# Optimization experiments

Measured on AMD Instinct MI355X. Metric: run time of the kernel, lower is better.

The kernel has to match this reference:

```python
import jax, jax.numpy as jnp
import numpy as np

NEG_INF = -1e30

def setup_inputs() -> dict:
    key = jax.random.key(0)
    ks = jax.random.split(key, 8)
    N, E = 4096, 16384
    Fn, Fe, Dn, De = 128, 64, 128, 64
    # xavier_uniform bound = sqrt(6/(fan_in+fan_out)); for 1-D params torch treats shape as (1, len)
    bn = np.sqrt(6.0 / (Fn + Dn))
    be = np.sqrt(6.0 / (Fe + De))
    return {
        "node_features": jax.random.normal(ks[0], (N, Fn), dtype=jnp.float32),
        "edge_features": jax.random.normal(ks[1], (E, Fe), dtype=jnp.float32),
        "adjacency_matrix": jax.random.randint(ks[2], (N, N), 0, 2, dtype=jnp.int32),
        "edge_adjacency_matrix": jax.random.randint(ks[3], (E, N), 0, 2, dtype=jnp.int32),
        "weight_node": jax.random.uniform(ks[4], (Fn, Dn), minval=-bn, maxval=bn, dtype=jnp.float32),
        "weight_edge": jax.random.uniform(ks[5], (Fe, De), minval=-be, maxval=be, dtype=jnp.float32),
        "parameter_vector_node": jax.random.uniform(ks[6], (2 * Dn,), minval=-1.0, maxval=1.0, dtype=jnp.float32),
        "parameter_vector_edge": jax.random.uniform(ks[7], (Dn + De,), minval=-1.0, maxval=1.0, dtype=jnp.float32),
    }


def reference(node_features, edge_features, adjacency_matrix, edge_adjacency_matrix,
              weight_node, weight_edge, parameter_vector_node, parameter_vector_edge):
    lrelu = jax.nn.leaky_relu  # default negative_slope=0.01, matches torch LeakyReLU
    Dn = weight_node.shape[1]

    h = node_features @ weight_node          # [N, Dn]
    he = edge_features @ weight_edge         # [E, De]

    # ---- node-level attention ----
    a_self, a_neigh = parameter_vector_node[:Dn], parameter_vector_node[Dn:]
    # score[i, j] = leaky_relu(a . cat(h_i, h_j)) for j a neighbor of i (adjacency[j, i] > 0)
    s_n = lrelu((h @ a_self)[:, None] + (h @ a_neigh)[None, :])   # [N, N]
    mask_n = adjacency_matrix.T > 0                                # [N, N], row i = neighbors of i
    coef_n = jax.nn.softmax(jnp.where(mask_n, s_n, NEG_INF), axis=1)
    coef_n = jnp.where(mask_n, coef_n, 0.0)
    deg_n = jnp.sum(mask_n, axis=1).astype(h.dtype)                # [N]
    means_n = (coef_n @ node_features) / deg_n[:, None]            # [N, Fn] (torch.mean divides by deg)
    out_n = lrelu(means_n @ weight_node)                           # [N, Dn]

    # ---- edge-level attention ----
    b_self, b_edge = parameter_vector_edge[:Dn], parameter_vector_edge[Dn:]
    s_e = lrelu((h @ b_self)[:, None] + (he @ b_edge)[None, :])    # [N, E]
    mask_e = edge_adjacency_matrix.T > 0                           # [N, E]
    coef_e = jax.nn.softmax(jnp.where(mask_e, s_e, NEG_INF), axis=1)
    coef_e = jnp.where(mask_e, coef_e, 0.0)
    deg_e = jnp.sum(mask_e, axis=1).astype(h.dtype)
    means_e = (coef_e @ edge_features) / deg_e[:, None]            # [N, Fe]
    out_e = lrelu(means_e @ weight_edge)                           # [N, De]

    return jnp.concatenate([out_n, out_e], axis=1)                 # [N, Dn+De]
```

## Files before the change

### kernel.cpp

```cpp
#include <hip/hip_runtime.h>

typedef short bf16x8 __attribute__((ext_vector_type(8)));
typedef float f32x4 __attribute__((ext_vector_type(4)));

#define N_NODES 4096
#define N_EDGES 16384
#define FN 128
#define FE 64
#define NJS 8
#define EJS 16

__device__ __forceinline__ float lrelu(float x) { return x >= 0.f ? x : 0.01f * x; }
__device__ __forceinline__ unsigned short f2bf(float f) {
    unsigned int x = __float_as_uint(f);
    return (unsigned short)((x + 0x7fffu + ((x >> 16) & 1u)) >> 16);
}

__global__ __launch_bounds__(256) void k_node_proj(
    const float* __restrict__ nf, const float* __restrict__ Wn,
    const float* __restrict__ pvn, const float* __restrict__ pve,
    float* __restrict__ alpha, float* __restrict__ beta, float* __restrict__ gamma) {
    __shared__ float row[4][FN];
    const int wv = threadIdx.x >> 6, ln = threadIdx.x & 63;
    const int i = blockIdx.x * 4 + wv;
    float2 r2 = *(const float2*)(nf + (size_t)i * FN + ln * 2);
    row[wv][ln * 2] = r2.x; row[wv][ln * 2 + 1] = r2.y;
    __syncthreads();
    float h0 = 0.f, h1 = 0.f;
#pragma unroll 8
    for (int k = 0; k < FN; ++k) {
        float nv = row[wv][k];
        float2 w2 = *(const float2*)(Wn + (size_t)k * FN + ln * 2);
        h0 = fmaf(nv, w2.x, h0); h1 = fmaf(nv, w2.y, h1);
    }
    float2 as = *(const float2*)(pvn + ln * 2);
    float2 an = *(const float2*)(pvn + FN + ln * 2);
    float2 bs = *(const float2*)(pve + ln * 2);
    float pa = h0 * as.x + h1 * as.y;
    float pb = h0 * an.x + h1 * an.y;
    float pg = h0 * bs.x + h1 * bs.y;
#pragma unroll
    for (int off = 32; off > 0; off >>= 1) {
        pa += __shfl_down(pa, off, 64);
        pb += __shfl_down(pb, off, 64);
        pg += __shfl_down(pg, off, 64);
    }
    if (ln == 0) { alpha[i] = pa; beta[i] = pb; gamma[i] = pg; }
}

__global__ __launch_bounds__(256) void k_edge_proj(
    const float* __restrict__ ef, const float* __restrict__ We,
    const float* __restrict__ pve, float* __restrict__ betaE) {
    __shared__ float row[4][FE];
    const int wv = threadIdx.x >> 6, ln = threadIdx.x & 63;
    const int e = blockIdx.x * 4 + wv;
    row[wv][ln] = ef[(size_t)e * FE + ln];
    __syncthreads();
    float h = 0.f;
#pragma unroll 8
    for (int k = 0; k < FE; ++k)
        h = fmaf(row[wv][k], We[(size_t)k * FE + ln], h);
    float p = h * pve[FN + ln];
#pragma unroll
    for (int off = 32; off > 0; off >>= 1) p += __shfl_down(p, off, 64);
    if (ln == 0) betaE[e] = p;
}

__global__ __launch_bounds__(256) void k_maxes(
    const float* __restrict__ beta, const float* __restrict__ betaE,
    float* __restrict__ maxes) {
    const float* src = blockIdx.x == 0 ? beta : betaE;
    const int n = blockIdx.x == 0 ? N_NODES : N_EDGES;
    float m = -3.0e38f;
    for (int t = threadIdx.x; t < n; t += 256) m = fmaxf(m, src[t]);
#pragma unroll
    for (int off = 32; off > 0; off >>= 1) m = fmaxf(m, __shfl_down(m, off, 64));
    __shared__ float sm[4];
    if ((threadIdx.x & 63) == 0) sm[threadIdx.x >> 6] = m;
    __syncthreads();
    if (threadIdx.x == 0)
        maxes[blockIdx.x] = fmaxf(fmaxf(sm[0], sm[1]), fmaxf(sm[2], sm[3]));
}

__global__ __launch_bounds__(256) void k_prep(
    const float* __restrict__ src, unsigned short* __restrict__ dst,
    const int J, const int F) {
    __shared__ float tile[64][65];
    const int t = threadIdx.x;
    const int j0 = blockIdx.x * 64, f0 = blockIdx.y * 64;
#pragma unroll
    for (int p = 0; p < 4; ++p) {
        int j = (t >> 4) + p * 16;
        float4 v = *(const float4*)(src + (size_t)(j0 + j) * F + f0 + (t & 15) * 4);
        tile[j][(t & 15) * 4 + 0] = v.x;
        tile[j][(t & 15) * 4 + 1] = v.y;
        tile[j][(t & 15) * 4 + 2] = v.z;
        tile[j][(t & 15) * 4 + 3] = v.w;
    }
    __syncthreads();
#pragma unroll
    for (int p = 0; p < 2; ++p) {
        int f = (t >> 3) + p * 32;
        int c = t & 7;
        bf16x8 v;
#pragma unroll
        for (int e = 0; e < 8; ++e) v[e] = (short)f2bf(tile[c * 8 + e][f]);
        *(bf16x8*)(dst + (size_t)(f0 + f) * J + j0 + c * 8) = v;
    }
}

__global__ __launch_bounds__(256) void k_node_att(
    const unsigned short* __restrict__ Xt,
    const int* __restrict__ adj,
    const float* __restrict__ alpha, const float* __restrict__ beta,
    const float* __restrict__ maxes,
    float* __restrict__ accP, float* __restrict__ zP, float* __restrict__ degP) {
    __shared__ unsigned short xlds[128 * 64];
    __shared__ unsigned short wlds[4 * 512];
    __shared__ float bb[512];
    __shared__ float zred[8][32];
    __shared__ float dred[8][32];
    const int t = threadIdx.x;
    const int i0 = blockIdx.x * 32;
    const int bj = blockIdx.y;
    const int j0 = bj * (N_NODES / NJS);
    const int il = t & 31;
    const int jg = t >> 5;
    const float a_i = alpha[i0 + il];
    const float m_i = lrelu(a_i + maxes[0]);
    if (t < 128) *(float4*)&bb[t * 4] = *(const float4*)(beta + j0 + t * 4);
    const int l = t & 63, wid = t >> 6;
    const int wm = wid >> 1, wn = wid & 1;
    const int l15 = l & 15, l4 = l >> 4;
    const int sf = t >> 3, sc = t & 7;
    const int xswz = (sc ^ (sf & 7)) * 8;
    const int wdst = ((jg >> 2) * 2 + (il >> 4)) * 512 + ((il & 15) + 16 * (jg & 3)) * 8;
    f32x4 acc[4] = {{0,0,0,0},{0,0,0,0},{0,0,0,0},{0,0,0,0}};
    float zacc = 0.f, dacc = 0.f;
    __syncthreads();
    for (int ks = 0; ks < 8; ++ks) {
        const int jb = ks * 64;
        const int* mp = adj + (size_t)(j0 + jb + jg * 8) * N_NODES + i0 + il;
        int mk[8];
#pragma unroll
        for (int e = 0; e < 8; ++e) mk[e] = mp[(size_t)e * N_NODES];
        const unsigned short* xs = Xt + (size_t)sf * N_NODES + j0 + jb + sc * 8;
        bf16x8 xv0 = *(const bf16x8*)(xs);
        bf16x8 xv1 = *(const bf16x8*)(xs + (size_t)32 * N_NODES);
        bf16x8 xv2 = *(const bf16x8*)(xs + (size_t)64 * N_NODES);
        bf16x8 xv3 = *(const bf16x8*)(xs + (size_t)96 * N_NODES);
        bf16x8 wfrag;
#pragma unroll
        for (int e = 0; e < 8; ++e) {
            float s = lrelu(a_i + bb[jb + jg * 8 + e]);
            float w = mk[e] > 0 ? __expf(s - m_i) : 0.f;
            zacc += w;
            dacc += (mk[e] > 0) ? 1.f : 0.f;
            wfrag[e] = (short)f2bf(w);
        }
        __syncthreads();
        *(bf16x8*)&xlds[(sf +  0) * 64 + xswz] = xv0;
        *(bf16x8*)&xlds[(sf + 32) * 64 + xswz] = xv1;
        *(bf16x8*)&xlds[(sf + 64) * 64 + xswz] = xv2;
        *(bf16x8*)&xlds[(sf + 96) * 64 + xswz] = xv3;
        *(bf16x8*)&wlds[wdst] = wfrag;
        __syncthreads();
#pragma unroll
        for (int kb = 0; kb < 2; ++kb) {
            bf16x8 b = *(const bf16x8*)&wlds[(kb * 2 + wn) * 512 + l * 8];
#pragma unroll
            for (int mi = 0; mi < 4; ++mi) {
                const int fr = wm * 64 + mi * 16 + l15;
                bf16x8 a = *(const bf16x8*)&xlds[fr * 64 + (((kb * 4 + l4) ^ (fr & 7)) * 8)];
                acc[mi] = __builtin_amdgcn_mfma_f32_16x16x32_bf16(a, b, acc[mi], 0, 0, 0);
            }
        }
    }
    zred[jg][il] = zacc;
    dred[jg][il] = dacc;
    __syncthreads();
    if (t < 32) {
        float z = 0.f, d = 0.f;
#pragma unroll
        for (int g = 0; g < 8; ++g) { z += zred[g][t]; d += dred[g][t]; }
        zP[bj * N_NODES + i0 + t] = z;
        degP[bj * N_NODES + i0 + t] = d;
    }
    const int ig = i0 + wn * 16 + l15;
#pragma unroll
    for (int mi = 0; mi < 4; ++mi) {
        const int fg = wm * 64 + mi * 16 + l4 * 4;
        *(f32x4*)(accP + ((size_t)bj * N_NODES + ig) * FN + fg) = acc[mi];
    }
}

__global__ __launch_bounds__(256) void k_edge_att(
    const unsigned short* __restrict__ Xt,
    const int* __restrict__ eadj,
    const float* __restrict__ gamma, const float* __restrict__ betaE,
    const float* __restrict__ maxes,
    float* __restrict__ accP, float* __restrict__ zP, float* __restrict__ degP) {
    __shared__ unsigned short xlds[64 * 32];
    __shared__ unsigned short wlds[4 * 512];
    __shared__ float bb[1024];
    __shared__ float zred[4][64];
    __shared__ float dred[4][64];
    const int t = threadIdx.x;
    const int i0 = blockIdx.x * 64;
    const int bj = blockIdx.y;
    const int j0 = bj * (N_EDGES / EJS);
    const int il = t & 63;
    const int jg = t >> 6;
    const float g_i = gamma[i0 + il];
    const float m_i = lrelu(g_i + maxes[1]);
    *(float4*)&bb[t * 4] = *(const float4*)(betaE + j0 + t * 4);
    const int l = t & 63, wid = t >> 6;
    const int wm = wid >> 1, wn = wid & 1;
    const int l15 = l & 15, l4 = l >> 4;
    const int sf = t >> 2, sc = t & 3;
    const unsigned short* xsrc = Xt + (size_t)sf * N_EDGES + j0 + sc * 8;
    const int xdst = sf * 32 + ((sc ^ (sf & 3)) * 8);
    const int wdst = (il >> 4) * 512 + ((il & 15) + 16 * jg) * 8;
    const int ar0 = (wm * 2) * 16 + l15;
    const int ar1 = (wm * 2 + 1) * 16 + l15;
    const int aad0 = ar0 * 32 + ((l4 ^ (ar0 & 3)) * 8);
    const int aad1 = ar1 * 32 + ((l4 ^ (ar1 & 3)) * 8);
    const int bad0 = (wn * 2) * 512 + l * 8;
    const int bad1 = (wn * 2 + 1) * 512 + l * 8;
    f32x4 acc00 = {0,0,0,0}, acc01 = {0,0,0,0}, acc10 = {0,0,0,0}, acc11 = {0,0,0,0};
    float zacc = 0.f, dacc = 0.f;
    __syncthreads();
    for (int ks = 0; ks < 32; ++ks) {
        const int jb = ks * 32;
        const int* mp = eadj + (size_t)(j0 + jb + jg * 8) * N_NODES + i0 + il;
        int mk[8];
#pragma unroll
        for (int e = 0; e < 8; ++e) mk[e] = mp[(size_t)e * N_NODES];
        bf16x8 xv = *(const bf16x8*)(xsrc + jb);
        bf16x8 wfrag;
#pragma unroll
        for (int e = 0; e < 8; ++e) {
            float s = lrelu(g_i + bb[jb + jg * 8 + e]);
            float w = mk[e] > 0 ? __expf(s - m_i) : 0.f;
            zacc += w;
            dacc += (mk[e] > 0) ? 1.f : 0.f;
            wfrag[e] = (short)f2bf(w);
        }
        __syncthreads();
        *(bf16x8*)&xlds[xdst] = xv;
        *(bf16x8*)&wlds[wdst] = wfrag;
        __syncthreads();
        bf16x8 a0 = *(const bf16x8*)&xlds[aad0];
        bf16x8 a1 = *(const bf16x8*)&xlds[aad1];
        bf16x8 b0 = *(const bf16x8*)&wlds[bad0];
        bf16x8 b1 = *(const bf16x8*)&wlds[bad1];
        acc00 = __builtin_amdgcn_mfma_f32_16x16x32_bf16(a0, b0, acc00, 0, 0, 0);
        acc01 = __builtin_amdgcn_mfma_f32_16x16x32_bf16(a0, b1, acc01, 0, 0, 0);
        acc10 = __builtin_amdgcn_mfma_f32_16x16x32_bf16(a1, b0, acc10, 0, 0, 0);
        acc11 = __builtin_amdgcn_mfma_f32_16x16x32_bf16(a1, b1, acc11, 0, 0, 0);
    }
    zred[jg][il] = zacc;
    dred[jg][il] = dacc;
    __syncthreads();
    if (t < 64) {
        float z = zred[0][t] + zred[1][t] + zred[2][t] + zred[3][t];
        float d = dred[0][t] + dred[1][t] + dred[2][t] + dred[3][t];
        zP[bj * N_NODES + i0 + t] = z;
        degP[bj * N_NODES + i0 + t] = d;
    }
    const size_t obase = (size_t)bj * N_NODES;
    {
        int ig0 = i0 + (wn * 2) * 16 + l15;
        int ig1 = i0 + (wn * 2 + 1) * 16 + l15;
        int fg0 = (wm * 2) * 16 + l4 * 4;
        int fg1 = (wm * 2 + 1) * 16 + l4 * 4;
        *(f32x4*)(accP + (obase + ig0) * FE + fg0) = acc00;
        *(f32x4*)(accP + (obase + ig1) * FE + fg0) = acc01;
        *(f32x4*)(accP + (obase + ig0) * FE + fg1) = acc10;
        *(f32x4*)(accP + (obase + ig1) * FE + fg1) = acc11;
    }
}

__global__ __launch_bounds__(256) void k_node_out(
    const float* __restrict__ accP, const float* __restrict__ zP,
    const float* __restrict__ degP, const float* __restrict__ Wn,
    float* __restrict__ out) {
    __shared__ float ml[4][FN];
    const int wv = threadIdx.x >> 6, ln = threadIdx.x & 63;
    const int i = blockIdx.x * 4 + wv;
    float s0 = 0.f, s1 = 0.f;
#pragma unroll
    for (int js = 0; js < NJS; ++js) {
        float2 v = *(const float2*)(accP + ((size_t)js * N_NODES + i) * FN + ln * 2);
        s0 += v.x; s1 += v.y;
    }
    float z = 0.f, d = 0.f;
#pragma unroll
    for (int js = 0; js < NJS; ++js) { z += zP[js * N_NODES + i]; d += degP[js * N_NODES + i]; }
    float zd = z * d;
    float inv = zd > 0.f ? 1.f / zd : 0.f;
    ml[wv][ln * 2] = s0 * inv; ml[wv][ln * 2 + 1] = s1 * inv;
    __syncthreads();
    float o0 = 0.f, o1 = 0.f;
#pragma unroll 8
    for (int k = 0; k < FN; ++k) {
        float mvv = ml[wv][k];
        float2 w2 = *(const float2*)(Wn + (size_t)k * FN + ln * 2);
        o0 = fmaf(mvv, w2.x, o0); o1 = fmaf(mvv, w2.y, o1);
    }
    out[(size_t)i * 192 + ln * 2] = lrelu(o0);
    out[(size_t)i * 192 + ln * 2 + 1] = lrelu(o1);
}

__global__ __launch_bounds__(256) void k_edge_out(
    const float* __restrict__ accP, const float* __restrict__ zP,
    const float* __restrict__ degP, const float* __restrict__ We,
    float* __restrict__ out) {
    __shared__ float ml[4][FE];
    const int wv = threadIdx.x >> 6, ln = threadIdx.x & 63;
    const int i = blockIdx.x * 4 + wv;
    float s = 0.f;
#pragma unroll
    for (int js = 0; js < EJS; ++js)
        s += accP[((size_t)js * N_NODES + i) * FE + ln];
    float z = 0.f, d = 0.f;
#pragma unroll
    for (int js = 0; js < EJS; ++js) { z += zP[js * N_NODES + i]; d += degP[js * N_NODES + i]; }
    float zd = z * d;
    float inv = zd > 0.f ? 1.f / zd : 0.f;
    ml[wv][ln] = s * inv;
    __syncthreads();
    float o = 0.f;
#pragma unroll 8
    for (int k = 0; k < FE; ++k)
        o = fmaf(ml[wv][k], We[(size_t)k * FE + ln], o);
    out[(size_t)i * 192 + 128 + ln] = lrelu(o);
}

extern "C" void kernel_launch(void* const* d_in, const int* in_sizes, int n_in,
                              void* d_out, int out_size, void* d_ws, size_t ws_size,
                              hipStream_t stream) {
    (void)in_sizes; (void)n_in; (void)out_size; (void)ws_size;
    const float* nf   = (const float*)d_in[0];
    const float* ef   = (const float*)d_in[1];
    const int*   adj  = (const int*)d_in[2];
    const int*   eadj = (const int*)d_in[3];
    const float* Wn   = (const float*)d_in[4];
    const float* We   = (const float*)d_in[5];
    const float* pvn  = (const float*)d_in[6];
    const float* pve  = (const float*)d_in[7];
    float* out = (float*)d_out;

    float* alpha = (float*)d_ws;
    float* beta  = alpha + 4096;
    float* gamma = beta + 4096;
    float* betaE = gamma + 4096;
    float* maxes = betaE + 16384;
    unsigned short* XtN = (unsigned short*)(maxes + 64);
    unsigned short* XtE = XtN + (size_t)FN * N_NODES;
    float* accN = (float*)(XtE + (size_t)FE * N_EDGES);
    float* zN   = accN + (size_t)NJS * N_NODES * FN;
    float* degN = zN + (size_t)NJS * N_NODES;
    float* accE = degN + (size_t)NJS * N_NODES;
    float* zE   = accE + (size_t)EJS * N_NODES * FE;
    float* degE = zE + (size_t)EJS * N_NODES;

    k_node_proj<<<N_NODES / 4, 256, 0, stream>>>(nf, Wn, pvn, pve, alpha, beta, gamma);
    k_edge_proj<<<N_EDGES / 4, 256, 0, stream>>>(ef, We, pve, betaE);
    k_maxes<<<2, 256, 0, stream>>>(beta, betaE, maxes);
    k_prep<<<dim3(N_NODES / 64, FN / 64), 256, 0, stream>>>(nf, XtN, N_NODES, FN);
    k_prep<<<dim3(N_EDGES / 64, FE / 64), 256, 0, stream>>>(ef, XtE, N_EDGES, FE);
    k_node_att<<<dim3(N_NODES / 32, NJS), 256, 0, stream>>>(XtN, adj, alpha, beta, maxes, accN, zN, degN);
    k_edge_att<<<dim3(N_NODES / 64, EJS), 256, 0, stream>>>(XtE, eadj, gamma, betaE, maxes, accE, zE, degE);
    k_node_out<<<N_NODES / 4, 256, 0, stream>>>(accN, zN, degN, Wn, out);
    k_edge_out<<<N_NODES / 4, 256, 0, stream>>>(accE, zE, degE, We, out);
}
```

Baseline: 165.4 us.

## Double-buffer LDS and prefetch next tile in node and edge attention kernels

Both attention kernels now use double-buffered shared-memory tiles and issue the global loads for the next K-step (adjacency mask and transposed features) before the barrier. This removes one __syncthreads per iteration and lets global memory latency overlap with the MFMA work. The edge kernel also widens its K-step from 32 to 64 edges, halving the iteration count and doing twice the MFMAs per barrier. In exchange it uses more LDS and registers, which may lower occupancy. The degree count now sums the raw mask values, which assumes the mask holds only 0 or 1.

```diff
diff --git a/kernel.cpp b/kernel.cpp
--- a/kernel.cpp
+++ b/kernel.cpp
@@ -115,8 +115,8 @@
     const float* __restrict__ alpha, const float* __restrict__ beta,
     const float* __restrict__ maxes,
     float* __restrict__ accP, float* __restrict__ zP, float* __restrict__ degP) {
-    __shared__ unsigned short xlds[128 * 64];
-    __shared__ unsigned short wlds[4 * 512];
+    __shared__ unsigned short xlds[2][128 * 64];
+    __shared__ unsigned short wlds[2][4 * 512];
     __shared__ float bb[512];
     __shared__ float zred[8][32];
     __shared__ float dred[8][32];
@@ -137,44 +137,59 @@
     const int wdst = ((jg >> 2) * 2 + (il >> 4)) * 512 + ((il & 15) + 16 * (jg & 3)) * 8;
     f32x4 acc[4] = {{0,0,0,0},{0,0,0,0},{0,0,0,0},{0,0,0,0}};
     float zacc = 0.f, dacc = 0.f;
-    __syncthreads();
+
+    const int* mp0 = adj + (size_t)(j0 + jg * 8) * N_NODES + i0 + il;
+    const unsigned short* xs0 = Xt + (size_t)sf * N_NODES + j0 + sc * 8;
+
+    int mk[8];
+#pragma unroll
+    for (int e = 0; e < 8; ++e) mk[e] = mp0[(size_t)e * N_NODES];
+    bf16x8 xv0 = *(const bf16x8*)(xs0);
+    bf16x8 xv1 = *(const bf16x8*)(xs0 + (size_t)32 * N_NODES);
+    bf16x8 xv2 = *(const bf16x8*)(xs0 + (size_t)64 * N_NODES);
+    bf16x8 xv3 = *(const bf16x8*)(xs0 + (size_t)96 * N_NODES);
+    __syncthreads();
+
+    int buf = 0;
     for (int ks = 0; ks < 8; ++ks) {
         const int jb = ks * 64;
-        const int* mp = adj + (size_t)(j0 + jb + jg * 8) * N_NODES + i0 + il;
-        int mk[8];
-#pragma unroll
-        for (int e = 0; e < 8; ++e) mk[e] = mp[(size_t)e * N_NODES];
-        const unsigned short* xs = Xt + (size_t)sf * N_NODES + j0 + jb + sc * 8;
-        bf16x8 xv0 = *(const bf16x8*)(xs);
-        bf16x8 xv1 = *(const bf16x8*)(xs + (size_t)32 * N_NODES);
-        bf16x8 xv2 = *(const bf16x8*)(xs + (size_t)64 * N_NODES);
-        bf16x8 xv3 = *(const bf16x8*)(xs + (size_t)96 * N_NODES);
         bf16x8 wfrag;
 #pragma unroll
         for (int e = 0; e < 8; ++e) {
             float s = lrelu(a_i + bb[jb + jg * 8 + e]);
             float w = mk[e] > 0 ? __expf(s - m_i) : 0.f;
             zacc += w;
-            dacc += (mk[e] > 0) ? 1.f : 0.f;
+            dacc += (float)mk[e];
             wfrag[e] = (short)f2bf(w);
         }
+        *(bf16x8*)&xlds[buf][(sf +  0) * 64 + xswz] = xv0;
+        *(bf16x8*)&xlds[buf][(sf + 32) * 64 + xswz] = xv1;
+        *(bf16x8*)&xlds[buf][(sf + 64) * 64 + xswz] = xv2;
+        *(bf16x8*)&xlds[buf][(sf + 96) * 64 + xswz] = xv3;
+        *(bf16x8*)&wlds[buf][wdst] = wfrag;
+        if (ks + 1 < 8) {
+            const int jbn = jb + 64;
+            const int* mp = mp0 + (size_t)jbn * N_NODES;
+#pragma unroll
+            for (int e = 0; e < 8; ++e) mk[e] = mp[(size_t)e * N_NODES];
+            const unsigned short* xs = xs0 + jbn;
+            xv0 = *(const bf16x8*)(xs);
+            xv1 = *(const bf16x8*)(xs + (size_t)32 * N_NODES);
+            xv2 = *(const bf16x8*)(xs + (size_t)64 * N_NODES);
+            xv3 = *(const bf16x8*)(xs + (size_t)96 * N_NODES);
+        }
         __syncthreads();
-        *(bf16x8*)&xlds[(sf +  0) * 64 + xswz] = xv0;
-        *(bf16x8*)&xlds[(sf + 32) * 64 + xswz] = xv1;
-        *(bf16x8*)&xlds[(sf + 64) * 64 + xswz] = xv2;
-        *(bf16x8*)&xlds[(sf + 96) * 64 + xswz] = xv3;
-        *(bf16x8*)&wlds[wdst] = wfrag;
-        __syncthreads();
 #pragma unroll
         for (int kb = 0; kb < 2; ++kb) {
-            bf16x8 b = *(const bf16x8*)&wlds[(kb * 2 + wn) * 512 + l * 8];
+            bf16x8 b = *(const bf16x8*)&wlds[buf][(kb * 2 + wn) * 512 + l * 8];
 #pragma unroll
             for (int mi = 0; mi < 4; ++mi) {
                 const int fr = wm * 64 + mi * 16 + l15;
-                bf16x8 a = *(const bf16x8*)&xlds[fr * 64 + (((kb * 4 + l4) ^ (fr & 7)) * 8)];
+                bf16x8 a = *(const bf16x8*)&xlds[buf][fr * 64 + (((kb * 4 + l4) ^ (fr & 7)) * 8)];
                 acc[mi] = __builtin_amdgcn_mfma_f32_16x16x32_bf16(a, b, acc[mi], 0, 0, 0);
             }
         }
+        buf ^= 1;
     }
     zred[jg][il] = zacc;
     dred[jg][il] = dacc;
@@ -200,8 +215,8 @@
     const float* __restrict__ gamma, const float* __restrict__ betaE,
     const float* __restrict__ maxes,
     float* __restrict__ accP, float* __restrict__ zP, float* __restrict__ degP) {
-    __shared__ unsigned short xlds[64 * 32];
-    __shared__ unsigned short wlds[4 * 512];
+    __shared__ unsigned short xlds[2][64 * 64];
+    __shared__ unsigned short wlds[2][8 * 512];
     __shared__ float bb[1024];
     __shared__ float zred[4][64];
     __shared__ float dred[4][64];
@@ -218,46 +233,68 @@
     const int wm = wid >> 1, wn = wid & 1;
     const int l15 = l & 15, l4 = l >> 4;
     const int sf = t >> 2, sc = t & 3;
+    const int xd0 = sf * 64 + ((sc       ^ (sf & 7)) * 8);
+    const int xd1 = sf * 64 + (((sc + 4) ^ (sf & 7)) * 8);
     const unsigned short* xsrc = Xt + (size_t)sf * N_EDGES + j0 + sc * 8;
-    const int xdst = sf * 32 + ((sc ^ (sf & 3)) * 8);
-    const int wdst = (il >> 4) * 512 + ((il & 15) + 16 * jg) * 8;
-    const int ar0 = (wm * 2) * 16 + l15;
-    const int ar1 = (wm * 2 + 1) * 16 + l15;
-    const int aad0 = ar0 * 32 + ((l4 ^ (ar0 & 3)) * 8);
-    const int aad1 = ar1 * 32 + ((l4 ^ (ar1 & 3)) * 8);
-    const int bad0 = (wn * 2) * 512 + l * 8;
-    const int bad1 = (wn * 2 + 1) * 512 + l * 8;
-    f32x4 acc00 = {0,0,0,0}, acc01 = {0,0,0,0}, acc10 = {0,0,0,0}, acc11 = {0,0,0,0};
+    const int wl = (il & 15) + 16 * jg;
+    const int nb = il >> 4;
+    f32x4 acc[2][2] = {{{0,0,0,0},{0,0,0,0}},{{0,0,0,0},{0,0,0,0}}};
     float zacc = 0.f, dacc = 0.f;
-    __syncthreads();
-    for (int ks = 0; ks < 32; ++ks) {
-        const int jb = ks * 32;
-        const int* mp = eadj + (size_t)(j0 + jb + jg * 8) * N_NODES + i0 + il;
-        int mk[8];
-#pragma unroll
-        for (int e = 0; e < 8; ++e) mk[e] = mp[(size_t)e * N_NODES];
-        bf16x8 xv = *(const bf16x8*)(xsrc + jb);
-        bf16x8 wfrag;
+
+    const int* mp0 = eadj + (size_t)(j0 + jg * 8) * N_NODES + i0 + il;
+
+    int mk0[8], mk1[8];
+#pragma unroll
+    for (int e = 0; e < 8; ++e) mk0[e] = mp0[(size_t)e * N_NODES];
+#pragma unroll
+    for (int e = 0; e < 8; ++e) mk1[e] = mp0[(size_t)(32 + e) * N_NODES];
+    bf16x8 xv0 = *(const bf16x8*)(xsrc);
+    bf16x8 xv1 = *(const bf16x8*)(xsrc + 32);
+    __syncthreads();
+
+    int buf = 0;
+    for (int ks = 0; ks < 16; ++ks) {
+        const int jb = ks * 64;
+        bf16x8 wf0, wf1;
 #pragma unroll
         for (int e = 0; e < 8; ++e) {
-            float s = lrelu(g_i + bb[jb + jg * 8 + e]);
-            float w = mk[e] > 0 ? __expf(s - m_i) : 0.f;
-            zacc += w;
-            dacc += (mk[e] > 0) ? 1.f : 0.f;
-            wfrag[e] = (short)f2bf(w);
+            float s0 = lrelu(g_i + bb[jb + jg * 8 + e]);
+            float w0 = mk0[e] > 0 ? __expf(s0 - m_i) : 0.f;
+            float s1 = lrelu(g_i + bb[jb + 32 + jg * 8 + e]);
+            float w1 = mk1[e] > 0 ? __expf(s1 - m_i) : 0.f;
+            zacc += w0 + w1;
+            dacc += (float)(mk0[e] + mk1[e]);
+            wf0[e] = (short)f2bf(w0);
+            wf1[e] = (short)f2bf(w1);
+        }
+        *(bf16x8*)&xlds[buf][xd0] = xv0;
+        *(bf16x8*)&xlds[buf][xd1] = xv1;
+        *(bf16x8*)&wlds[buf][(0 * 4 + nb) * 512 + wl * 8] = wf0;
+        *(bf16x8*)&wlds[buf][(1 * 4 + nb) * 512 + wl * 8] = wf1;
+        if (ks + 1 < 16) {
+            const int jbn = jb + 64;
+            const int* mp = mp0 + (size_t)jbn * N_NODES;
+#pragma unroll
+            for (int e = 0; e < 8; ++e) mk0[e] = mp[(size_t)e * N_NODES];
+#pragma unroll
+            for (int e = 0; e < 8; ++e) mk1[e] = mp[(size_t)(32 + e) * N_NODES];
+            xv0 = *(const bf16x8*)(xsrc + jbn);
+            xv1 = *(const bf16x8*)(xsrc + jbn + 32);
         }
         __syncthreads();
-        *(bf16x8*)&xlds[xdst] = xv;
-        *(bf16x8*)&wlds[wdst] = wfrag;
-        __syncthreads();
-        bf16x8 a0 = *(const bf16x8*)&xlds[aad0];
-        bf16x8 a1 = *(const bf16x8*)&xlds[aad1];
-        bf16x8 b0 = *(const bf16x8*)&wlds[bad0];
-        bf16x8 b1 = *(const bf16x8*)&wlds[bad1];
-        acc00 = __builtin_amdgcn_mfma_f32_16x16x32_bf16(a0, b0, acc00, 0, 0, 0);
-        acc01 = __builtin_amdgcn_mfma_f32_16x16x32_bf16(a0, b1, acc01, 0, 0, 0);
-        acc10 = __builtin_amdgcn_mfma_f32_16x16x32_bf16(a1, b0, acc10, 0, 0, 0);
-        acc11 = __builtin_amdgcn_mfma_f32_16x16x32_bf16(a1, b1, acc11, 0, 0, 0);
+#pragma unroll
+        for (int kb = 0; kb < 2; ++kb) {
+            bf16x8 b0 = *(const bf16x8*)&wlds[buf][(kb * 4 + wn * 2 + 0) * 512 + l * 8];
+            bf16x8 b1 = *(const bf16x8*)&wlds[buf][(kb * 4 + wn * 2 + 1) * 512 + l * 8];
+#pragma unroll
+            for (int mi = 0; mi < 2; ++mi) {
+                const int fr = wm * 32 + mi * 16 + l15;
+                bf16x8 a = *(const bf16x8*)&xlds[buf][fr * 64 + (((kb * 4 + l4) ^ (fr & 7)) * 8)];
+                acc[mi][0] = __builtin_amdgcn_mfma_f32_16x16x32_bf16(a, b0, acc[mi][0], 0, 0, 0);
+                acc[mi][1] = __builtin_amdgcn_mfma_f32_16x16x32_bf16(a, b1, acc[mi][1], 0, 0, 0);
+            }
+        }
+        buf ^= 1;
     }
     zred[jg][il] = zacc;
     dred[jg][il] = dacc;
@@ -269,15 +306,14 @@
         degP[bj * N_NODES + i0 + t] = d;
     }
     const size_t obase = (size_t)bj * N_NODES;
-    {
-        int ig0 = i0 + (wn * 2) * 16 + l15;
-        int ig1 = i0 + (wn * 2 + 1) * 16 + l15;
-        int fg0 = (wm * 2) * 16 + l4 * 4;
-        int fg1 = (wm * 2 + 1) * 16 + l4 * 4;
-        *(f32x4*)(accP + (obase + ig0) * FE + fg0) = acc00;
-        *(f32x4*)(accP + (obase + ig1) * FE + fg0) = acc01;
-        *(f32x4*)(accP + (obase + ig0) * FE + fg1) = acc10;
-        *(f32x4*)(accP + (obase + ig1) * FE + fg1) = acc11;
+#pragma unroll
+    for (int mi = 0; mi < 2; ++mi) {
+#pragma unroll
+        for (int p = 0; p < 2; ++p) {
+            int ig = i0 + wn * 32 + p * 16 + l15;
+            int fg = wm * 32 + mi * 16 + l4 * 4;
+            *(f32x4*)(accP + (obase + ig) * FE + fg) = acc[mi][p];
+        }
     }
 }
 
```

Measured after the change: 165.1 us. Within noise of the previous version (-0.2%).

## Bit-pack adjacency masks, fuse front kernels, drop LDS staging in attention

Applied to the files above, without the earlier changes.

Adds a pass that packs the int32 adjacency and edge-adjacency matrices into 64-bit ballot bitmasks. This pass is merged with the node/edge projection and bf16 feature-prep work into one front kernel. The attention kernels now read the packed mask bits and a new blocked bf16 feature layout straight from global memory into MFMA operands, with no LDS staging or block barriers. The full int32 matrices are still read once, but the attention stage fetches far fewer mask bytes and skips syncs. The trade-off is repeated global reads of the feature operands across waves and extra workspace.

```diff
diff --git a/kernel.cpp b/kernel.cpp
--- a/kernel.cpp
+++ b/kernel.cpp
@@ -2,6 +2,7 @@
 
 typedef short bf16x8 __attribute__((ext_vector_type(8)));
 typedef float f32x4 __attribute__((ext_vector_type(4)));
+typedef unsigned long long u64;
 
 #define N_NODES 4096
 #define N_EDGES 16384
@@ -9,6 +10,14 @@
 #define FE 64
 #define NJS 8
 #define EJS 16
+#define WPR 64
+
+#define PACK_BLOCKS ((N_NODES + N_EDGES) / 4)
+#define NPROJ_BLOCKS (N_NODES / 4)
+#define EPROJ_BLOCKS (N_EDGES / 4)
+#define PREPN_BLOCKS (N_NODES / 64)
+#define PREPE_BLOCKS (N_EDGES / 64)
+#define FRONT_BLOCKS (PACK_BLOCKS + NPROJ_BLOCKS + EPROJ_BLOCKS + PREPN_BLOCKS + PREPE_BLOCKS)
 
 __device__ __forceinline__ float lrelu(float x) { return x >= 0.f ? x : 0.01f * x; }
 __device__ __forceinline__ unsigned short f2bf(float f) {
@@ -16,54 +25,116 @@
     return (unsigned short)((x + 0x7fffu + ((x >> 16) & 1u)) >> 16);
 }
 
-__global__ __launch_bounds__(256) void k_node_proj(
-    const float* __restrict__ nf, const float* __restrict__ Wn,
+__device__ __forceinline__ void prep_b(
+    const float* __restrict__ src, unsigned short* __restrict__ dst,
+    int j0, int F, int lf, float* tile ) {
+    const int t = threadIdx.x;
+    const int P = F + 1;
+    for (int it = 0; it < (F >> 4); ++it) {
+        int idx = (it * 256 + t) * 4;
+        int j = idx >> lf, f = idx & (F - 1);
+        float4 v = *(const float4*)(src + (size_t)(j0 + j) * F + f);
+        tile[j * P + f + 0] = v.x; tile[j * P + f + 1] = v.y;
+        tile[j * P + f + 2] = v.z; tile[j * P + f + 3] = v.w;
+    }
+    __syncthreads();
+    for (int it = 0; it < (F >> 5); ++it) {
+        int c = it * 256 + t;
+        int jo = c >> lf, f = c & (F - 1);
+        bf16x8 v;
+#pragma unroll
+        for (int e = 0; e < 8; ++e) v[e] = (short)f2bf(tile[(jo * 8 + e) * P + f]);
+        *(bf16x8*)(dst + (((size_t)(j0 >> 3) + jo) * F + f) * 8) = v;
+    }
+}
+
+__global__ __launch_bounds__(256) void k_front(
+    const float* __restrict__ nf, const float* __restrict__ ef,
+    const int* __restrict__ adj, const int* __restrict__ eadj,
+    const float* __restrict__ Wn, const float* __restrict__ We,
     const float* __restrict__ pvn, const float* __restrict__ pve,
-    float* __restrict__ alpha, float* __restrict__ beta, float* __restrict__ gamma) {
-    __shared__ float row[4][FN];
+    u64* __restrict__ adjP, u64* __restrict__ eadjP,
+    float* __restrict__ alpha, float* __restrict__ beta, float* __restrict__ gamma,
+    float* __restrict__ betaE,
+    unsigned short* __restrict__ XbN, unsigned short* __restrict__ XbE) {
+    __shared__ float smem[8256];
+    int bx = blockIdx.x;
     const int wv = threadIdx.x >> 6, ln = threadIdx.x & 63;
-    const int i = blockIdx.x * 4 + wv;
-    float2 r2 = *(const float2*)(nf + (size_t)i * FN + ln * 2);
-    row[wv][ln * 2] = r2.x; row[wv][ln * 2 + 1] = r2.y;
-    __syncthreads();
-    float h0 = 0.f, h1 = 0.f;
+
+    if (bx < PACK_BLOCKS) {
+        const int row = bx * 4 + wv;
+        const int* src;
+        u64* dst;
+        if (row < N_EDGES) {
+            src = eadj + (size_t)row * N_NODES;
+            dst = eadjP + (size_t)row * WPR;
+        } else {
+            src = adj + (size_t)(row - N_EDGES) * N_NODES;
+            dst = adjP + (size_t)(row - N_EDGES) * WPR;
+        }
+#pragma unroll 4
+        for (int chunk = 0; chunk < 16; ++chunk) {
+            int4 v = *(const int4*)(src + chunk * 256 + ln * 4);
+            u64 b0 = __ballot(v.x > 0);
+            u64 b1 = __ballot(v.y > 0);
+            u64 b2 = __ballot(v.z > 0);
+            u64 b3 = __ballot(v.w > 0);
+            if (ln < 4) dst[chunk * 4 + ln] = (ln == 0) ? b0 : (ln == 1) ? b1 : (ln == 2) ? b2 : b3;
+        }
+        return;
+    }
+    bx -= PACK_BLOCKS;
+    if (bx < NPROJ_BLOCKS) {
+        float* row = smem;
+        const int i = bx * 4 + wv;
+        float2 r2 = *(const float2*)(nf + (size_t)i * FN + ln * 2);
+        row[wv * FN + ln * 2] = r2.x; row[wv * FN + ln * 2 + 1] = r2.y;
+        __syncthreads();
+        float h0 = 0.f, h1 = 0.f;
 #pragma unroll 8
-    for (int k = 0; k < FN; ++k) {
-        float nv = row[wv][k];
-        float2 w2 = *(const float2*)(Wn + (size_t)k * FN + ln * 2);
-        h0 = fmaf(nv, w2.x, h0); h1 = fmaf(nv, w2.y, h1);
-    }
-    float2 as = *(const float2*)(pvn + ln * 2);
-    float2 an = *(const float2*)(pvn + FN + ln * 2);
-    float2 bs = *(const float2*)(pve + ln * 2);
-    float pa = h0 * as.x + h1 * as.y;
-    float pb = h0 * an.x + h1 * an.y;
-    float pg = h0 * bs.x + h1 * bs.y;
-#pragma unroll
-    for (int off = 32; off > 0; off >>= 1) {
-        pa += __shfl_down(pa, off, 64);
-        pb += __shfl_down(pb, off, 64);
-        pg += __shfl_down(pg, off, 64);
-    }
-    if (ln == 0) { alpha[i] = pa; beta[i] = pb; gamma[i] = pg; }
-}
-
-__global__ __launch_bounds__(256) void k_edge_proj(
-    const float* __restrict__ ef, const float* __restrict__ We,
-    const float* __restrict__ pve, float* __restrict__ betaE) {
-    __shared__ float row[4][FE];
-    const int wv = threadIdx.x >> 6, ln = threadIdx.x & 63;
-    const int e = blockIdx.x * 4 + wv;
-    row[wv][ln] = ef[(size_t)e * FE + ln];
-    __syncthreads();
-    float h = 0.f;
+        for (int k = 0; k < FN; ++k) {
+            float nv = row[wv * FN + k];
+            float2 w2 = *(const float2*)(Wn + (size_t)k * FN + ln * 2);
+            h0 = fmaf(nv, w2.x, h0); h1 = fmaf(nv, w2.y, h1);
+        }
+        float2 as = *(const float2*)(pvn + ln * 2);
+        float2 an = *(const float2*)(pvn + FN + ln * 2);
+        float2 bs = *(const float2*)(pve + ln * 2);
+        float pa = h0 * as.x + h1 * as.y;
+        float pb = h0 * an.x + h1 * an.y;
+        float pg = h0 * bs.x + h1 * bs.y;
+#pragma unroll
+        for (int off = 32; off > 0; off >>= 1) {
+            pa += __shfl_down(pa, off, 64);
+            pb += __shfl_down(pb, off, 64);
+            pg += __shfl_down(pg, off, 64);
+        }
+        if (ln == 0) { alpha[i] = pa; beta[i] = pb; gamma[i] = pg; }
+        return;
+    }
+    bx -= NPROJ_BLOCKS;
+    if (bx < EPROJ_BLOCKS) {
+        float* row = smem;
+        const int e = bx * 4 + wv;
+        row[wv * FE + ln] = ef[(size_t)e * FE + ln];
+        __syncthreads();
+        float h = 0.f;
 #pragma unroll 8
-    for (int k = 0; k < FE; ++k)
-        h = fmaf(row[wv][k], We[(size_t)k * FE + ln], h);
-    float p = h * pve[FN + ln];
-#pragma unroll
-    for (int off = 32; off > 0; off >>= 1) p += __shfl_down(p, off, 64);
-    if (ln == 0) betaE[e] = p;
+        for (int k = 0; k < FE; ++k)
+            h = fmaf(row[wv * FE + k], We[(size_t)k * FE + ln], h);
+        float p = h * pve[FN + ln];
+#pragma unroll
+        for (int off = 32; off > 0; off >>= 1) p += __shfl_down(p, off, 64);
+        if (ln == 0) betaE[e] = p;
+        return;
+    }
+    bx -= EPROJ_BLOCKS;
+    if (bx < PREPN_BLOCKS) {
+        prep_b(nf, XbN, bx * 64, FN, 7, smem);
+        return;
+    }
+    bx -= PREPN_BLOCKS;
+    prep_b(ef, XbE, bx * 64, FE, 6, smem);
 }
 
 __global__ __launch_bounds__(256) void k_maxes(
@@ -72,7 +143,10 @@
     const float* src = blockIdx.x == 0 ? beta : betaE;
     const int n = blockIdx.x == 0 ? N_NODES : N_EDGES;
     float m = -3.0e38f;
-    for (int t = threadIdx.x; t < n; t += 256) m = fmaxf(m, src[t]);
+    for (int t = threadIdx.x * 4; t < n; t += 1024) {
+        float4 v = *(const float4*)(src + t);
+        m = fmaxf(m, fmaxf(fmaxf(v.x, v.y), fmaxf(v.z, v.w)));
+    }
 #pragma unroll
     for (int off = 32; off > 0; off >>= 1) m = fmaxf(m, __shfl_down(m, off, 64));
     __shared__ float sm[4];
@@ -82,203 +156,120 @@
         maxes[blockIdx.x] = fmaxf(fmaxf(sm[0], sm[1]), fmaxf(sm[2], sm[3]));
 }
 
-__global__ __launch_bounds__(256) void k_prep(
-    const float* __restrict__ src, unsigned short* __restrict__ dst,
-    const int J, const int F) {
-    __shared__ float tile[64][65];
-    const int t = threadIdx.x;
-    const int j0 = blockIdx.x * 64, f0 = blockIdx.y * 64;
-#pragma unroll
-    for (int p = 0; p < 4; ++p) {
-        int j = (t >> 4) + p * 16;
-        float4 v = *(const float4*)(src + (size_t)(j0 + j) * F + f0 + (t & 15) * 4);
-        tile[j][(t & 15) * 4 + 0] = v.x;
-        tile[j][(t & 15) * 4 + 1] = v.y;
-        tile[j][(t & 15) * 4 + 2] = v.z;
-        tile[j][(t & 15) * 4 + 3] = v.w;
-    }
-    __syncthreads();
-#pragma unroll
-    for (int p = 0; p < 2; ++p) {
-        int f = (t >> 3) + p * 32;
-        int c = t & 7;
-        bf16x8 v;
-#pragma unroll
-        for (int e = 0; e < 8; ++e) v[e] = (short)f2bf(tile[c * 8 + e][f]);
-        *(bf16x8*)(dst + (size_t)(f0 + f) * J + j0 + c * 8) = v;
-    }
-}
-
 __global__ __launch_bounds__(256) void k_node_att(
-    const unsigned short* __restrict__ Xt,
-    const int* __restrict__ adj,
+    const unsigned short* __restrict__ Xb,
+    const u64* __restrict__ adjP,
     const float* __restrict__ alpha, const float* __restrict__ beta,
     const float* __restrict__ maxes,
     float* __restrict__ accP, float* __restrict__ zP, float* __restrict__ degP) {
-    __shared__ unsigned short xlds[128 * 64];
-    __shared__ unsigned short wlds[4 * 512];
-    __shared__ float bb[512];
-    __shared__ float zred[8][32];
-    __shared__ float dred[8][32];
-    const int t = threadIdx.x;
-    const int i0 = blockIdx.x * 32;
+    const int t = threadIdx.x, l = t & 63, wid = t >> 6;
+    const int l15 = l & 15, lq = l >> 4;
     const int bj = blockIdx.y;
     const int j0 = bj * (N_NODES / NJS);
-    const int il = t & 31;
-    const int jg = t >> 5;
-    const float a_i = alpha[i0 + il];
+    const int i0 = blockIdx.x * 64 + wid * 16;
+    const int i = i0 + l15;
+    const float a_i = alpha[i];
     const float m_i = lrelu(a_i + maxes[0]);
-    if (t < 128) *(float4*)&bb[t * 4] = *(const float4*)(beta + j0 + t * 4);
-    const int l = t & 63, wid = t >> 6;
-    const int wm = wid >> 1, wn = wid & 1;
-    const int l15 = l & 15, l4 = l >> 4;
-    const int sf = t >> 3, sc = t & 7;
-    const int xswz = (sc ^ (sf & 7)) * 8;
-    const int wdst = ((jg >> 2) * 2 + (il >> 4)) * 512 + ((il & 15) + 16 * (jg & 3)) * 8;
-    f32x4 acc[4] = {{0,0,0,0},{0,0,0,0},{0,0,0,0},{0,0,0,0}};
+    const int wbase = (i0 >> 8) * 4 + (l15 & 3);
+    const int mbit = (i >> 2) & 63;
+    f32x4 acc[8] = {};
     float zacc = 0.f, dacc = 0.f;
-    __syncthreads();
-    for (int ks = 0; ks < 8; ++ks) {
-        const int jb = ks * 64;
-        const int* mp = adj + (size_t)(j0 + jb + jg * 8) * N_NODES + i0 + il;
-        int mk[8];
-#pragma unroll
-        for (int e = 0; e < 8; ++e) mk[e] = mp[(size_t)e * N_NODES];
-        const unsigned short* xs = Xt + (size_t)sf * N_NODES + j0 + jb + sc * 8;
-        bf16x8 xv0 = *(const bf16x8*)(xs);
-        bf16x8 xv1 = *(const bf16x8*)(xs + (size_t)32 * N_NODES);
-        bf16x8 xv2 = *(const bf16x8*)(xs + (size_t)64 * N_NODES);
-        bf16x8 xv3 = *(const bf16x8*)(xs + (size_t)96 * N_NODES);
-        bf16x8 wfrag;
+    const u64* mp0 = adjP + (size_t)j0 * WPR + wbase + (size_t)(lq * 8) * WPR;
+    const unsigned short* xb0 = Xb + (((size_t)(j0 >> 3) + lq) * FN + l15) * 8;
+    const float* bb0 = beta + j0 + lq * 8;
+
+    for (int ks = 0; ks < 16; ++ks) {
+        const int jb = ks * 32;
+        u64 mw[8];
+        const u64* mp = mp0 + (size_t)jb * WPR;
+#pragma unroll
+        for (int e = 0; e < 8; ++e) mw[e] = mp[(size_t)e * WPR];
+        float4 b0 = *(const float4*)(bb0 + jb);
+        float4 b1 = *(const float4*)(bb0 + jb + 4);
+        float bv[8] = {b0.x, b0.y, b0.z, b0.w, b1.x, b1.y, b1.z, b1.w};
+        bf16x8 wf;
 #pragma unroll
         for (int e = 0; e < 8; ++e) {
-            float s = lrelu(a_i + bb[jb + jg * 8 + e]);
-            float w = mk[e] > 0 ? __expf(s - m_i) : 0.f;
-            zacc += w;
-            dacc += (mk[e] > 0) ? 1.f : 0.f;
-            wfrag[e] = (short)f2bf(w);
-        }
-        __syncthreads();
-        *(bf16x8*)&xlds[(sf +  0) * 64 + xswz] = xv0;
-        *(bf16x8*)&xlds[(sf + 32) * 64 + xswz] = xv1;
-        *(bf16x8*)&xlds[(sf + 64) * 64 + xswz] = xv2;
-        *(bf16x8*)&xlds[(sf + 96) * 64 + xswz] = xv3;
-        *(bf16x8*)&wlds[wdst] = wfrag;
-        __syncthreads();
-#pragma unroll
-        for (int kb = 0; kb < 2; ++kb) {
-            bf16x8 b = *(const bf16x8*)&wlds[(kb * 2 + wn) * 512 + l * 8];
-#pragma unroll
-            for (int mi = 0; mi < 4; ++mi) {
-                const int fr = wm * 64 + mi * 16 + l15;
-                bf16x8 a = *(const bf16x8*)&xlds[fr * 64 + (((kb * 4 + l4) ^ (fr & 7)) * 8)];
-                acc[mi] = __builtin_amdgcn_mfma_f32_16x16x32_bf16(a, b, acc[mi], 0, 0, 0);
-            }
-        }
-    }
-    zred[jg][il] = zacc;
-    dred[jg][il] = dacc;
-    __syncthreads();
-    if (t < 32) {
-        float z = 0.f, d = 0.f;
-#pragma unroll
-        for (int g = 0; g < 8; ++g) { z += zred[g][t]; d += dred[g][t]; }
-        zP[bj * N_NODES + i0 + t] = z;
-        degP[bj * N_NODES + i0 + t] = d;
-    }
-    const int ig = i0 + wn * 16 + l15;
-#pragma unroll
-    for (int mi = 0; mi < 4; ++mi) {
-        const int fg = wm * 64 + mi * 16 + l4 * 4;
-        *(f32x4*)(accP + ((size_t)bj * N_NODES + ig) * FN + fg) = acc[mi];
-    }
+            int mk = (int)((mw[e] >> mbit) & 1);
+            float s = lrelu(a_i + bv[e]);
+            float w = mk ? __expf(s - m_i) : 0.f;
+            zacc += w; dacc += (float)mk;
+            wf[e] = (short)f2bf(w);
+        }
+        const unsigned short* xa = xb0 + (size_t)(jb >> 3) * (FN * 8);
+#pragma unroll
+        for (int mi = 0; mi < 8; ++mi) {
+            bf16x8 a = *(const bf16x8*)(xa + mi * 128);
+            acc[mi] = __builtin_amdgcn_mfma_f32_16x16x32_bf16(a, wf, acc[mi], 0, 0, 0);
+        }
+    }
+    zacc += __shfl_xor(zacc, 16, 64); zacc += __shfl_xor(zacc, 32, 64);
+    dacc += __shfl_xor(dacc, 16, 64); dacc += __shfl_xor(dacc, 32, 64);
+    if (l < 16) {
+        zP[bj * N_NODES + i] = zacc;
+        degP[bj * N_NODES + i] = dacc;
+    }
+#pragma unroll
+    for (int mi = 0; mi < 8; ++mi)
+        *(f32x4*)(accP + ((size_t)bj * N_NODES + i) * FN + mi * 16 + lq * 4) = acc[mi];
 }
 
 __global__ __launch_bounds__(256) void k_edge_att(
-    const unsigned short* __restrict__ Xt,
-    const int* __restrict__ eadj,
+    const unsigned short* __restrict__ Xb,
+    const u64* __restrict__ eadjP,
     const float* __restrict__ gamma, const float* __restrict__ betaE,
     const float* __restrict__ maxes,
     float* __restrict__ accP, float* __restrict__ zP, float* __restrict__ degP) {
-    __shared__ unsigned short xlds[64 * 32];
-    __shared__ unsigned short wlds[4 * 512];
-    __shared__ float bb[1024];
-    __shared__ float zred[4][64];
-    __shared__ float dred[4][64];
-    const int t = threadIdx.x;
-    const int i0 = blockIdx.x * 64;
+    const int t = threadIdx.x, l = t & 63, wid = t >> 6;
+    const int l15 = l & 15, lq = l >> 4;
     const int bj = blockIdx.y;
     const int j0 = bj * (N_EDGES / EJS);
-    const int il = t & 63;
-    const int jg = t >> 6;
-    const float g_i = gamma[i0 + il];
-    const float m_i = lrelu(g_i + maxes[1]);
-    *(float4*)&bb[t * 4] = *(const float4*)(betaE + j0 + t * 4);
-    const int l = t & 63, wid = t >> 6;
-    const int wm = wid >> 1, wn = wid & 1;
-    const int l15 = l & 15, l4 = l >> 4;
-    const int sf = t >> 2, sc = t & 3;
-    const unsigned short* xsrc = Xt + (size_t)sf * N_EDGES + j0 + sc * 8;
-    const int xdst = sf * 32 + ((sc ^ (sf & 3)) * 8);
-    const int wdst = (il >> 4) * 512 + ((il & 15) + 16 * jg) * 8;
-    const int ar0 = (wm * 2) * 16 + l15;
-    const int ar1 = (wm * 2 + 1) * 16 + l15;
-    const int aad0 = ar0 * 32 + ((l4 ^ (ar0 & 3)) * 8);
-    const int aad1 = ar1 * 32 + ((l4 ^ (ar1 & 3)) * 8);
-    const int bad0 = (wn * 2) * 512 + l * 8;
-    const int bad1 = (wn * 2 + 1) * 512 + l * 8;
-    f32x4 acc00 = {0,0,0,0}, acc01 = {0,0,0,0}, acc10 = {0,0,0,0}, acc11 = {0,0,0,0};
+    const int i0 = blockIdx.x * 64 + wid * 16;
+    const int i = i0 + l15;
+    const float a_i = gamma[i];
+    const float m_i = lrelu(a_i + maxes[1]);
+    const int wbase = (i0 >> 8) * 4 + (l15 & 3);
+    const int mbit = (i >> 2) & 63;
+    f32x4 acc[4] = {};
     float zacc = 0.f, dacc = 0.f;
-    __syncthreads();
+    const u64* mp0 = eadjP + (size_t)j0 * WPR + wbase + (size_t)(lq * 8) * WPR;
+    const unsigned short* xb0 = Xb + (((size_t)(j0 >> 3) + lq) * FE + l15) * 8;
+    const float* bb0 = betaE + j0 + lq * 8;
+
     for (int ks = 0; ks < 32; ++ks) {
         const int jb = ks * 32;
-        const int* mp = eadj + (size_t)(j0 + jb + jg * 8) * N_NODES + i0 + il;
-        int mk[8];
-#pragma unroll
-        for (int e = 0; e < 8; ++e) mk[e] = mp[(size_t)e * N_NODES];
-        bf16x8 xv = *(const bf16x8*)(xsrc + jb);
-        bf16x8 wfrag;
+        u64 mw[8];
+        const u64* mp = mp0 + (size_t)jb * WPR;
+#pragma unroll
+        for (int e = 0; e < 8; ++e) mw[e] = mp[(size_t)e * WPR];
+        float4 b0 = *(const float4*)(bb0 + jb);
+        float4 b1 = *(const float4*)(bb0 + jb + 4);
+        float bv[8] = {b0.x, b0.y, b0.z, b0.w, b1.x, b1.y, b1.z, b1.w};
+        bf16x8 wf;
 #pragma unroll
         for (int e = 0; e < 8; ++e) {
-            float s = lrelu(g_i + bb[jb + jg * 8 + e]);
-            float w = mk[e] > 0 ? __expf(s - m_i) : 0.f;
-            zacc += w;
-            dacc += (mk[e] > 0) ? 1.f : 0.f;
-            wfrag[e] = (short)f2bf(w);
-        }
-        __syncthreads();
-        *(bf16x8*)&xlds[xdst] = xv;
-        *(bf16x8*)&wlds[wdst] = wfrag;
-        __syncthreads();
-        bf16x8 a0 = *(const bf16x8*)&xlds[aad0];
-        bf16x8 a1 = *(const bf16x8*)&xlds[aad1];
-        bf16x8 b0 = *(const bf16x8*)&wlds[bad0];
-        bf16x8 b1 = *(const bf16x8*)&wlds[bad1];
-        acc00 = __builtin_amdgcn_mfma_f32_16x16x32_bf16(a0, b0, acc00, 0, 0, 0);
-        acc01 = __builtin_amdgcn_mfma_f32_16x16x32_bf16(a0, b1, acc01, 0, 0, 0);
-        acc10 = __builtin_amdgcn_mfma_f32_16x16x32_bf16(a1, b0, acc10, 0, 0, 0);
-        acc11 = __builtin_amdgcn_mfma_f32_16x16x32_bf16(a1, b1, acc11, 0, 0, 0);
-    }
-    zred[jg][il] = zacc;
-    dred[jg][il] = dacc;
-    __syncthreads();
-    if (t < 64) {
-        float z = zred[0][t] + zred[1][t] + zred[2][t] + zred[3][t];
-        float d = dred[0][t] + dred[1][t] + dred[2][t] + dred[3][t];
-        zP[bj * N_NODES + i0 + t] = z;
-        degP[bj * N_NODES + i0 + t] = d;
-    }
-    const size_t obase = (size_t)bj * N_NODES;
-    {
-        int ig0 = i0 + (wn * 2) * 16 + l15;
-        int ig1 = i0 + (wn * 2 + 1) * 16 + l15;
-        int fg0 = (wm * 2) * 16 + l4 * 4;
-        int fg1 = (wm * 2 + 1) * 16 + l4 * 4;
-        *(f32x4*)(accP + (obase + ig0) * FE + fg0) = acc00;
-        *(f32x4*)(accP + (obase + ig1) * FE + fg0) = acc01;
-        *(f32x4*)(accP + (obase + ig0) * FE + fg1) = acc10;
-        *(f32x4*)(accP + (obase + ig1) * FE + fg1) = acc11;
-    }
+            int mk = (int)((mw[e] >> mbit) & 1);
+            float s = lrelu(a_i + bv[e]);
+            float w = mk ? __expf(s - m_i) : 0.f;
+            zacc += w; dacc += (float)mk;
+            wf[e] = (short)f2bf(w);
+        }
+        const unsigned short* xa = xb0 + (size_t)(jb >> 3) * (FE * 8);
+#pragma unroll
+        for (int mi = 0; mi < 4; ++mi) {
+            bf16x8 a = *(const bf16x8*)(xa + mi * 128);
+            acc[mi] = __builtin_amdgcn_mfma_f32_16x16x32_bf16(a, wf, acc[mi], 0, 0, 0);
+        }
+    }
+    zacc += __shfl_xor(zacc, 16, 64); zacc += __shfl_xor(zacc, 32, 64);
+    dacc += __shfl_xor(dacc, 16, 64); dacc += __shfl_xor(dacc, 32, 64);
+    if (l < 16) {
+        zP[bj * N_NODES + i] = zacc;
+        degP[bj * N_NODES + i] = dacc;
+    }
+#pragma unroll
+    for (int mi = 0; mi < 4; ++mi)
+        *(f32x4*)(accP + ((size_t)bj * N_NODES + i) * FE + mi * 16 + lq * 4) = acc[mi];
 }
 
 __global__ __launch_bounds__(256) void k_node_out(
@@ -351,27 +342,27 @@
     const float* pve  = (const float*)d_in[7];
     float* out = (float*)d_out;
 
-    float* alpha = (float*)d_ws;
+    u64* adjP  = (u64*)d_ws;
+    u64* eadjP = adjP + (size_t)N_NODES * WPR;
+    float* alpha = (float*)(eadjP + (size_t)N_EDGES * WPR);
     float* beta  = alpha + 4096;
     float* gamma = beta + 4096;
     float* betaE = gamma + 4096;
     float* maxes = betaE + 16384;
-    unsigned short* XtN = (unsigned short*)(maxes + 64);
-    unsigned short* XtE = XtN + (size_t)FN * N_NODES;
-    float* accN = (float*)(XtE + (size_t)FE * N_EDGES);
+    unsigned short* XbN = (unsigned short*)(maxes + 64);
+    unsigned short* XbE = XbN + (size_t)(N_NODES / 8) * FN * 8;
+    float* accN = (float*)(XbE + (size_t)(N_EDGES / 8) * FE * 8);
     float* zN   = accN + (size_t)NJS * N_NODES * FN;
     float* degN = zN + (size_t)NJS * N_NODES;
     float* accE = degN + (size_t)NJS * N_NODES;
     float* zE   = accE + (size_t)EJS * N_NODES * FE;
     float* degE = zE + (size_t)EJS * N_NODES;
 
-    k_node_proj<<<N_NODES / 4, 256, 0, stream>>>(nf, Wn, pvn, pve, alpha, beta, gamma);
-    k_edge_proj<<<N_EDGES / 4, 256, 0, stream>>>(ef, We, pve, betaE);
+    k_front<<<FRONT_BLOCKS, 256, 0, stream>>>(nf, ef, adj, eadj, Wn, We, pvn, pve,
+                                              adjP, eadjP, alpha, beta, gamma, betaE, XbN, XbE);
     k_maxes<<<2, 256, 0, stream>>>(beta, betaE, maxes);
-    k_prep<<<dim3(N_NODES / 64, FN / 64), 256, 0, stream>>>(nf, XtN, N_NODES, FN);
-    k_prep<<<dim3(N_EDGES / 64, FE / 64), 256, 0, stream>>>(ef, XtE, N_EDGES, FE);
-    k_node_att<<<dim3(N_NODES / 32, NJS), 256, 0, stream>>>(XtN, adj, alpha, beta, maxes, accN, zN, degN);
-    k_edge_att<<<dim3(N_NODES / 64, EJS), 256, 0, stream>>>(XtE, eadj, gamma, betaE, maxes, accE, zE, degE);
+    k_node_att<<<dim3(N_NODES / 64, NJS), 256, 0, stream>>>(XbN, adjP, alpha, beta, maxes, accN, zN, degN);
+    k_edge_att<<<dim3(N_NODES / 64, EJS), 256, 0, stream>>>(XbE, eadjP, gamma, betaE, maxes, accE, zE, degE);
     k_node_out<<<N_NODES / 4, 256, 0, stream>>>(accN, zN, degN, Wn, out);
     k_edge_out<<<N_NODES / 4, 256, 0, stream>>>(accE, zE, degE, We, out);
 }
```

Measured after the change: 210.5 us. 1.27x slower.
